# Performance work log

Measured on AMD Instinct MI355X. Metric: run time of the kernel, lower is better.

## Reference

```python
import jax, jax.numpy as jnp
import numpy as np

N_NODES = 100000


def sage_conv(x, src, dst, Wl, bl, Wr):
    # PyG SAGEConv (aggr='mean'): out = lin_l(mean_{j in N(i)} x_j) + lin_r(x_i)
    msg = x[src]                                                   # [E, d] gather
    agg = jax.ops.segment_sum(msg, dst, num_segments=N_NODES)      # [N, d]
    cnt = jax.ops.segment_sum(jnp.ones((src.shape[0], 1), x.dtype), dst,
                              num_segments=N_NODES)                # [N, 1]
    mean = agg / jnp.maximum(cnt, 1.0)
    return mean @ Wl + bl + x @ Wr


def setup_inputs() -> dict:
    key = jax.random.key(0)
    ks = jax.random.split(key, 9)
    N, E, D_IN = N_NODES, 3200000, 64
    x = jax.random.normal(ks[0], (N, D_IN), dtype=jnp.float32)
    edge_index = jax.random.randint(ks[1], (2, E), 0, N, dtype=jnp.int64)

    def glorot(k, fan_in, fan_out):
        lim = float(np.sqrt(6.0 / (fan_in + fan_out)))
        return jax.random.uniform(k, (fan_in, fan_out), jnp.float32, -lim, lim)

    return {
        "x": x,
        "edge_index": edge_index,
        "W1l": glorot(ks[2], D_IN, 64), "b1": jnp.zeros((64,), jnp.float32),
        "W1r": glorot(ks[3], D_IN, 64),
        "W2l": glorot(ks[4], 64, 32), "b2": jnp.zeros((32,), jnp.float32),
        "W2r": glorot(ks[5], 64, 32),
        "W3l": glorot(ks[6], 32, 1), "b3": jnp.zeros((1,), jnp.float32),
        "W3r": glorot(ks[7], 32, 1),
    }


def reference(x, edge_index, W1l, b1, W1r, W2l, b2, W2r, W3l, b3, W3r):
    src, dst = edge_index[0], edge_index[1]
    h = jax.nn.relu(sage_conv(x, src, dst, W1l, b1, W1r))   # dropout: eval mode (identity)
    h = jax.nn.relu(sage_conv(h, src, dst, W2l, b2, W2r))
    h = sage_conv(h, src, dst, W3l, b3, W3r)
    return jax.nn.sigmoid(h)                                # [N, 1]
```

## Files before the change

kernel.cpp:

```cpp
#include <hip/hip_runtime.h>
#include <math.h>

#define NN 100000
#define NB 391
#define BT 8192
#define CAP 12288

typedef float vfloat2 __attribute__((ext_vector_type(2)));
typedef short short8 __attribute__((ext_vector_type(8)));
typedef float floatx4 __attribute__((ext_vector_type(4)));

__device__ __forceinline__ unsigned short f2bf(float f) {
    unsigned int u = __float_as_uint(f);
    u += 0x7fffu + ((u >> 16) & 1u);
    return (unsigned short)(u >> 16);
}

__device__ __forceinline__ unsigned char f2fp8(float f) {
    const int p = __builtin_amdgcn_cvt_pk_fp8_f32(f, f, 0, false);
    return (unsigned char)(p & 0xFF);
}
template <bool HI>
__device__ __forceinline__ vfloat2 fp8pk2(unsigned int w) {
    return __builtin_amdgcn_cvt_pk_f32_fp8((int)w, HI);
}

template <int D_IN, int CL, int CR, int NPB, int FUSE_IN>
__global__ void __launch_bounds__(256)
mlp_mfma_kernel(const float* __restrict__ in0,
                const float* __restrict__ in1,
                const float* __restrict__ Wl,
                const float* __restrict__ Wr,
                const float* __restrict__ bias,
                unsigned char* __restrict__ yout,
                float* __restrict__ zout,
                int n_nodes) {
    constexpr int COLS = CL + CR;
    constexpr int CT = COLS / 16;
    constexpr int KT = D_IN / 32;
    constexpr int NT = NPB / 16;
    constexpr int KG = D_IN / 8;
    __shared__ short sA[NT * KT * 64 * 8];
    __shared__ short sB[CT * KT * 64 * 8];
    __shared__ float sBias[CR];
    const int t = threadIdx.x;
    const int node0 = blockIdx.x * NPB;

    for (int i = t; i < NPB * KG; i += 256) {
        const int nl = i / KG, kg = i % KG;
        const int n = node0 + nl;
        float v[8];
        if (n < n_nodes) {
            const float4* p = (const float4*)(in0 + (long long)n * D_IN + kg * 8);
            float4 a0 = p[0], a1 = p[1];
            if (FUSE_IN) {
                const float4* q = (const float4*)(in1 + (long long)n * D_IN + kg * 8);
                const float4 b0 = q[0], b1 = q[1];
                a0.x = fmaxf(a0.x + b0.x, 0.f); a0.y = fmaxf(a0.y + b0.y, 0.f);
                a0.z = fmaxf(a0.z + b0.z, 0.f); a0.w = fmaxf(a0.w + b0.w, 0.f);
                a1.x = fmaxf(a1.x + b1.x, 0.f); a1.y = fmaxf(a1.y + b1.y, 0.f);
                a1.z = fmaxf(a1.z + b1.z, 0.f); a1.w = fmaxf(a1.w + b1.w, 0.f);
            }
            v[0] = a0.x; v[1] = a0.y; v[2] = a0.z; v[3] = a0.w;
            v[4] = a1.x; v[5] = a1.y; v[6] = a1.z; v[7] = a1.w;
        } else {
#pragma unroll
            for (int j = 0; j < 8; ++j) v[j] = 0.f;
        }
        short8 s;
#pragma unroll
        for (int j = 0; j < 8; ++j) s[j] = (short)f2bf(v[j]);
        const int nt = nl >> 4, m = nl & 15, kt = kg >> 2, quad = kg & 3;
        ((short8*)sA)[(nt * KT + kt) * 64 + quad * 16 + m] = s;
    }
    for (int i = t; i < CT * KT * 64; i += 256) {
        const int ct = i / (KT * 64);
        const int rem = i % (KT * 64);
        const int kt = rem / 64, L = rem % 64;
        const int c = ct * 16 + (L & 15);
        const int k0 = kt * 32 + (L >> 4) * 8;
        short8 s;
#pragma unroll
        for (int j = 0; j < 8; ++j) {
            const int k = k0 + j;
            const float w = (c < CL) ? Wl[k * CL + c] : Wr[k * CR + (c - CL)];
            s[j] = (short)f2bf(w);
        }
        ((short8*)sB)[i] = s;
    }
    for (int i = t; i < CR; i += 256) sBias[i] = bias[i];
    __syncthreads();

    const int w = t >> 6, lane = t & 63;
    short8 Bf[CT][KT];
#pragma unroll
    for (int ct = 0; ct < CT; ++ct)
#pragma unroll
        for (int kt = 0; kt < KT; ++kt)
            Bf[ct][kt] = ((short8*)sB)[(ct * KT + kt) * 64 + lane];
    const int col = lane & 15, quad = lane >> 4;
#pragma unroll
    for (int nti = 0; nti < NT / 4; ++nti) {
        const int nt = w * (NT / 4) + nti;
        short8 A[KT];
#pragma unroll
        for (int kt = 0; kt < KT; ++kt)
            A[kt] = ((short8*)sA)[(nt * KT + kt) * 64 + lane];
        const int nodeb = node0 + nt * 16 + quad * 4;
#pragma unroll
        for (int ct = 0; ct < CT; ++ct) {
            floatx4 acc = {0.f, 0.f, 0.f, 0.f};
#pragma unroll
            for (int kt = 0; kt < KT; ++kt)
                acc = __builtin_amdgcn_mfma_f32_16x16x32_bf16(A[kt], Bf[ct][kt], acc, 0, 0, 0);
            const int gc = ct * 16 + col;
#pragma unroll
            for (int r = 0; r < 4; ++r) {
                const int node = nodeb + r;
                if (node < n_nodes) {
                    if (gc < CL) yout[(long long)node * CL + gc] = f2fp8(acc[r]);
                    else zout[(long long)node * CR + (gc - CL)] = acc[r] + sBias[gc - CL];
                }
            }
        }
    }
}

template <int D_IN>
__global__ void __launch_bounds__(256)
mlp3_kernel(const float* __restrict__ mean,
            const float* __restrict__ z,
            const float* __restrict__ W3l,
            const float* __restrict__ W3r,
            const float* __restrict__ b3,
            float* __restrict__ y,
            float* __restrict__ z3, int n_nodes) {
    __shared__ float swl[D_IN], swr[D_IN];
    const int t = threadIdx.x;
    if (t < D_IN) { swl[t] = W3l[t]; swr[t] = W3r[t]; }
    __syncthreads();
    const int n = blockIdx.x * 256 + t;
    if (n >= n_nodes) return;
    const float4* pm = (const float4*)(mean + (long long)n * D_IN);
    const float4* pz = (const float4*)(z + (long long)n * D_IN);
    float accl = 0.f, accr = 0.f;
#pragma unroll
    for (int q = 0; q < D_IN / 4; ++q) {
        const float4 m4 = pm[q];
        const float4 z4 = pz[q];
        const float h0 = fmaxf(m4.x + z4.x, 0.f);
        const float h1 = fmaxf(m4.y + z4.y, 0.f);
        const float h2 = fmaxf(m4.z + z4.z, 0.f);
        const float h3 = fmaxf(m4.w + z4.w, 0.f);
        accl += h0 * swl[4 * q] + h1 * swl[4 * q + 1] + h2 * swl[4 * q + 2] + h3 * swl[4 * q + 3];
        accr += h0 * swr[4 * q] + h1 * swr[4 * q + 1] + h2 * swr[4 * q + 2] + h3 * swr[4 * q + 3];
    }
    y[n] = accl;
    z3[n] = accr + b3[0];
}

template <int D>
__global__ void agg_mean_fp8_kernel(const unsigned int* __restrict__ yb,
                                    const int* __restrict__ row_ptr,
                                    const int* __restrict__ ssrc,
                                    const float* __restrict__ inv_deg,
                                    float* __restrict__ mean, int n_nodes) {
    constexpr int G = D / 16;
    constexpr int NPB = 256 / G;
    const int g = threadIdx.x / G;
    const int lane = threadIdx.x % G;
    const int n = blockIdx.x * NPB + g;
    if (n >= n_nodes) return;
    const int s0 = row_ptr[n], s1 = row_ptr[n + 1];
    const uint4* yv = (const uint4*)yb;
    float acc[16];
#pragma unroll
    for (int i = 0; i < 16; ++i) acc[i] = 0.f;
    int e = s0;
    for (; e + 4 <= s1; e += 4) {
        uint4 v[4];
        v[0] = yv[(long long)ssrc[e] * G + lane];
        v[1] = yv[(long long)ssrc[e + 1] * G + lane];
        v[2] = yv[(long long)ssrc[e + 2] * G + lane];
        v[3] = yv[(long long)ssrc[e + 3] * G + lane];
#pragma unroll
        for (int q = 0; q < 4; ++q) {
            const unsigned int wx = v[q].x, wy = v[q].y, wz = v[q].z, ww = v[q].w;
            vfloat2 p;
            p = fp8pk2<false>(wx); acc[0]  += p.x; acc[1]  += p.y;
            p = fp8pk2<true>(wx);  acc[2]  += p.x; acc[3]  += p.y;
            p = fp8pk2<false>(wy); acc[4]  += p.x; acc[5]  += p.y;
            p = fp8pk2<true>(wy);  acc[6]  += p.x; acc[7]  += p.y;
            p = fp8pk2<false>(wz); acc[8]  += p.x; acc[9]  += p.y;
            p = fp8pk2<true>(wz);  acc[10] += p.x; acc[11] += p.y;
            p = fp8pk2<false>(ww); acc[12] += p.x; acc[13] += p.y;
            p = fp8pk2<true>(ww);  acc[14] += p.x; acc[15] += p.y;
        }
    }
    for (; e < s1; ++e) {
        const uint4 v = yv[(long long)ssrc[e] * G + lane];
        vfloat2 p;
        p = fp8pk2<false>(v.x); acc[0]  += p.x; acc[1]  += p.y;
        p = fp8pk2<true>(v.x);  acc[2]  += p.x; acc[3]  += p.y;
        p = fp8pk2<false>(v.y); acc[4]  += p.x; acc[5]  += p.y;
        p = fp8pk2<true>(v.y);  acc[6]  += p.x; acc[7]  += p.y;
        p = fp8pk2<false>(v.z); acc[8]  += p.x; acc[9]  += p.y;
        p = fp8pk2<true>(v.z);  acc[10] += p.x; acc[11] += p.y;
        p = fp8pk2<false>(v.w); acc[12] += p.x; acc[13] += p.y;
        p = fp8pk2<true>(v.w);  acc[14] += p.x; acc[15] += p.y;
    }
    const float inv = inv_deg[n];
    float4* mv = (float4*)mean;
    const long long base = (long long)n * (D / 4) + lane * 4;
#pragma unroll
    for (int q = 0; q < 4; ++q)
        mv[base + q] = make_float4(acc[4 * q] * inv, acc[4 * q + 1] * inv,
                                   acc[4 * q + 2] * inv, acc[4 * q + 3] * inv);
}

__global__ void agg_d1_sig_kernel(const float* __restrict__ y,
                                  const int* __restrict__ row_ptr,
                                  const int* __restrict__ ssrc,
                                  const float* __restrict__ inv_deg,
                                  const float* __restrict__ z3,
                                  float* __restrict__ out, int n_nodes) {
    const int wave = threadIdx.x >> 6;
    const int lane = threadIdx.x & 63;
    const int n = blockIdx.x * 4 + wave;
    if (n >= n_nodes) return;
    const int s0 = row_ptr[n], s1 = row_ptr[n + 1];
    float acc = 0.f;
    for (int e = s0 + lane; e < s1; e += 64) acc += y[ssrc[e]];
    for (int off = 32; off > 0; off >>= 1) acc += __shfl_down(acc, off, 64);
    if (lane == 0) {
        const float v = acc * inv_deg[n] + z3[n];
        out[n] = 1.0f / (1.0f + expf(-v));
    }
}

__global__ void bucket_hist_kernel(const int* __restrict__ dst,
                                   int* __restrict__ bcnt, int n_edges) {
    __shared__ int lh[NB];
    for (int i = threadIdx.x; i < NB; i += 256) lh[i] = 0;
    __syncthreads();
    const int stride = gridDim.x * 256;
    for (int i = blockIdx.x * 256 + threadIdx.x; i < n_edges; i += stride)
        atomicAdd(&lh[dst[i] >> 8], 1);
    __syncthreads();
    for (int i = threadIdx.x; i < NB; i += 256)
        if (lh[i]) atomicAdd(&bcnt[i], lh[i]);
}

__global__ void __launch_bounds__(512)
bucket_scan_kernel(const int* __restrict__ bcnt, int* __restrict__ boffs,
                   int* __restrict__ bcursor) {
    __shared__ int s[512];
    const int t = threadIdx.x;
    const int v = (t < NB) ? bcnt[t] : 0;
    s[t] = v;
    __syncthreads();
    for (int off = 1; off < 512; off <<= 1) {
        const int tmp = (t >= off) ? s[t - off] : 0;
        __syncthreads();
        s[t] += tmp;
        __syncthreads();
    }
    const int excl = s[t] - v;
    if (t <= NB) boffs[t] = excl;
    if (t < NB) bcursor[t] = excl;
}

__global__ void __launch_bounds__(512)
bin_edges_kernel(const int* __restrict__ src, const int* __restrict__ dst,
                 int* __restrict__ bcursor, unsigned int* __restrict__ binned,
                 int n_edges) {
    __shared__ unsigned int stage[BT];
    __shared__ unsigned short sbkt[BT];
    __shared__ int lhist[512], lscan[512], lstart[512], gbase[512], lcur[512];
    const int t = threadIdx.x;
    const int e0 = blockIdx.x * BT;
    const int count = min(BT, n_edges - e0);
    lhist[t] = 0;
    __syncthreads();
    for (int i = t; i < count; i += 512) atomicAdd(&lhist[dst[e0 + i] >> 8], 1);
    __syncthreads();
    const int v = lhist[t];
    lscan[t] = v;
    __syncthreads();
    for (int off = 1; off < 512; off <<= 1) {
        const int tmp = (t >= off) ? lscan[t - off] : 0;
        __syncthreads();
        lscan[t] += tmp;
        __syncthreads();
    }
    const int excl = lscan[t] - v;
    lstart[t] = excl;
    lcur[t] = excl;
    if (t < NB && v > 0) gbase[t] = atomicAdd(&bcursor[t], v);
    __syncthreads();
    for (int i = t; i < count; i += 512) {
        const int d = dst[e0 + i];
        const int b = d >> 8;
        const int p = atomicAdd(&lcur[b], 1);
        stage[p] = (unsigned int)src[e0 + i] | ((unsigned int)(d & 255) << 17);
        sbkt[p] = (unsigned short)b;
    }
    __syncthreads();
    for (int i = t; i < count; i += 512) {
        const int b = sbkt[i];
        binned[gbase[b] + (i - lstart[b])] = stage[i];
    }
}

__global__ void __launch_bounds__(1024)
csr_sort_kernel(const unsigned int* __restrict__ binned,
                const int* __restrict__ boffs,
                int* __restrict__ ssrc, int* __restrict__ row_ptr,
                float* __restrict__ inv_deg, int n_nodes, int n_edges) {
    __shared__ int stage[CAP];
    __shared__ int hist[256];
    __shared__ int lexcl[256];
    __shared__ int lcur[256];
    const int t = threadIdx.x;
    const int b = blockIdx.x;
    const int s0 = boffs[b], s1 = boffs[b + 1];
    const int count = s1 - s0;
    if (t < 256) hist[t] = 0;
    __syncthreads();
    for (int i = t; i < count; i += 1024)
        atomicAdd(&hist[binned[s0 + i] >> 17], 1);
    __syncthreads();
    if (t < 256) lexcl[t] = hist[t];
    __syncthreads();
    for (int off = 1; off < 256; off <<= 1) {
        int tmp = 0;
        if (t < 256 && t >= off) tmp = lexcl[t - off];
        __syncthreads();
        if (t < 256) lexcl[t] += tmp;
        __syncthreads();
    }
    if (t < 256) {
        const int excl = lexcl[t] - hist[t];
        lcur[t] = excl;
        const int n = (b << 8) + t;
        if (n < n_nodes) {
            row_ptr[n] = s0 + excl;
            inv_deg[n] = 1.0f / (float)max(hist[t], 1);
        }
    }
    if (b == NB - 1 && t == 0) row_ptr[n_nodes] = n_edges;
    __syncthreads();
    for (int i = t; i < count; i += 1024) {
        const unsigned int v = binned[s0 + i];
        const int p = atomicAdd(&lcur[v >> 17], 1);
        if (p < CAP) stage[p] = (int)(v & 0x1FFFFu);
    }
    __syncthreads();
    for (int i = t; i < count; i += 1024) ssrc[s0 + i] = stage[i];
}

extern "C" void kernel_launch(void* const* d_in, const int* in_sizes, int n_in,
                              void* d_out, int out_size, void* d_ws, size_t ws_size,
                              hipStream_t stream) {
    const float* x = (const float*)d_in[0];
    const int* edge_index = (const int*)d_in[1];
    const float* W1l = (const float*)d_in[2];
    const float* b1  = (const float*)d_in[3];
    const float* W1r = (const float*)d_in[4];
    const float* W2l = (const float*)d_in[5];
    const float* b2  = (const float*)d_in[6];
    const float* W2r = (const float*)d_in[7];
    const float* W3l = (const float*)d_in[8];
    const float* b3  = (const float*)d_in[9];
    const float* W3r = (const float*)d_in[10];
    float* out = (float*)d_out;

    const int E = in_sizes[1] / 2;
    const int* src = edge_index;
    const int* dst = edge_index + E;

    float* bufY    = (float*)d_ws;
    float* meanB   = bufY + 32LL * NN;
    float* z1      = meanB + 64LL * NN;
    float* z2      = z1 + 64LL * NN;
    float* z3      = z2 + 32LL * NN;
    float* inv_deg = z3 + NN;
    int* bcnt      = (int*)(inv_deg + NN);
    int* boffs     = bcnt + NB;
    int* bcursor   = boffs + NB + 1;
    int* row_ptr   = bcursor + NB;
    int* ssrc      = row_ptr + NN + 1;
    unsigned int* binned = (unsigned int*)z1;

    const int ntiles = (E + BT - 1) / BT;

    (void)hipMemsetAsync(bcnt, 0, NB * sizeof(int), stream);
    bucket_hist_kernel<<<512, 256, 0, stream>>>(dst, bcnt, E);
    bucket_scan_kernel<<<1, 512, 0, stream>>>(bcnt, boffs, bcursor);
    bin_edges_kernel<<<ntiles, 512, 0, stream>>>(src, dst, bcursor, binned, E);
    csr_sort_kernel<<<NB, 1024, 0, stream>>>(binned, boffs, ssrc, row_ptr, inv_deg, NN, E);

    mlp_mfma_kernel<64, 64, 64, 128, 0><<<(NN + 127) / 128, 256, 0, stream>>>(
        x, nullptr, W1l, W1r, b1, (unsigned char*)bufY, z1, NN);
    agg_mean_fp8_kernel<64><<<(NN + 63) / 64, 256, 0, stream>>>(
        (const unsigned int*)bufY, row_ptr, ssrc, inv_deg, meanB, NN);

    mlp_mfma_kernel<64, 32, 32, 128, 1><<<(NN + 127) / 128, 256, 0, stream>>>(
        meanB, z1, W2l, W2r, b2, (unsigned char*)bufY, z2, NN);
    agg_mean_fp8_kernel<32><<<(NN + 127) / 128, 256, 0, stream>>>(
        (const unsigned int*)bufY, row_ptr, ssrc, inv_deg, meanB, NN);

    float* y3 = bufY;
    mlp3_kernel<32><<<(NN + 255) / 256, 256, 0, stream>>>(
        meanB, z2, W3l, W3r, b3, y3, z3, NN);

    agg_d1_sig_kernel<<<(NN + 3) / 4, 256, 0, stream>>>(
        y3, row_ptr, ssrc, inv_deg, z3, out, NN);
}
```

Baseline: 310.0 us.

## Fuse CSR build kernels into one cooperative kernel with grid syncs

Replaces the memset and four separate CSR-construction kernels (bucket histogram, scan, edge binning, per-bucket sort) with a single cooperative kernel of NB blocks that separates the phases with grid-wide syncs and reuses a shared-memory union. The aim is to remove launch overhead and inter-kernel gaps. In exchange, the grid is limited to 391 blocks of 512 threads, so the binning and sort phases run with less parallelism than before (the sort drops from 1024 to 512 threads per block). Grid syncs also add their own cost, and the large shared-memory union may cut occupancy.

After: 482.8 us. 55.8% more time.

```diff
diff --git a/kernel.cpp b/kernel.cpp
--- a/kernel.cpp
+++ b/kernel.cpp
@@ -1,5 +1,8 @@
 #include <hip/hip_runtime.h>
+#include <hip/hip_cooperative_groups.h>
 #include <math.h>
+
+namespace cg = cooperative_groups;
 
 #define NN 100000
 #define NB 391
@@ -23,6 +26,134 @@
 template <bool HI>
 __device__ __forceinline__ vfloat2 fp8pk2(unsigned int w) {
     return __builtin_amdgcn_cvt_pk_f32_fp8((int)w, HI);
+}
+
+union BuildSmem {
+    struct { int lh[NB]; } hist;
+    struct { int s[512]; } scan;
+    struct {
+        unsigned int stage[BT];
+        unsigned short sbkt[BT];
+        int lhist[512], lscan[512], lstart[512], gbase[512], lcur[512];
+    } bin;
+    struct { int stage[CAP]; int hist[256]; int lexcl[256]; int lcur[256]; } sort;
+};
+
+__global__ void __launch_bounds__(512)
+build_csr_coop(const int* __restrict__ src, const int* __restrict__ dst,
+               int* __restrict__ bcnt, int* __restrict__ boffs,
+               int* __restrict__ bcursor, unsigned int* __restrict__ binned,
+               int* __restrict__ ssrc, int* __restrict__ row_ptr,
+               float* __restrict__ inv_deg, int n_nodes, int n_edges) {
+    cg::grid_group grid = cg::this_grid();
+    __shared__ BuildSmem u;
+    const int t = threadIdx.x;
+    const int nb = gridDim.x;
+
+    for (int i = blockIdx.x * 512 + t; i < NB; i += nb * 512) bcnt[i] = 0;
+    grid.sync();
+
+    for (int i = t; i < NB; i += 512) u.hist.lh[i] = 0;
+    __syncthreads();
+    for (int e = blockIdx.x * 512 + t; e < n_edges; e += nb * 512)
+        atomicAdd(&u.hist.lh[dst[e] >> 8], 1);
+    __syncthreads();
+    for (int i = t; i < NB; i += 512) {
+        const int v = u.hist.lh[i];
+        if (v) atomicAdd(&bcnt[i], v);
+    }
+    grid.sync();
+
+    if (blockIdx.x == 0) {
+        const int v = (t < NB) ? bcnt[t] : 0;
+        u.scan.s[t] = v;
+        __syncthreads();
+        for (int off = 1; off < 512; off <<= 1) {
+            const int tmp = (t >= off) ? u.scan.s[t - off] : 0;
+            __syncthreads();
+            u.scan.s[t] += tmp;
+            __syncthreads();
+        }
+        const int excl = u.scan.s[t] - v;
+        if (t <= NB) boffs[t] = excl;
+        if (t < NB) bcursor[t] = excl;
+    }
+    grid.sync();
+
+    for (int tile = blockIdx.x; (long long)tile * BT < n_edges; tile += nb) {
+        const int e0 = tile * BT;
+        const int count = min(BT, n_edges - e0);
+        u.bin.lhist[t] = 0;
+        __syncthreads();
+        for (int i = t; i < count; i += 512) atomicAdd(&u.bin.lhist[dst[e0 + i] >> 8], 1);
+        __syncthreads();
+        const int v = u.bin.lhist[t];
+        u.bin.lscan[t] = v;
+        __syncthreads();
+        for (int off = 1; off < 512; off <<= 1) {
+            const int tmp = (t >= off) ? u.bin.lscan[t - off] : 0;
+            __syncthreads();
+            u.bin.lscan[t] += tmp;
+            __syncthreads();
+        }
+        const int excl = u.bin.lscan[t] - v;
+        u.bin.lstart[t] = excl;
+        u.bin.lcur[t] = excl;
+        if (t < NB && v > 0) u.bin.gbase[t] = atomicAdd(&bcursor[t], v);
+        __syncthreads();
+        for (int i = t; i < count; i += 512) {
+            const int d = dst[e0 + i];
+            const int b = d >> 8;
+            const int p = atomicAdd(&u.bin.lcur[b], 1);
+            u.bin.stage[p] = (unsigned int)src[e0 + i] | ((unsigned int)(d & 255) << 17);
+            u.bin.sbkt[p] = (unsigned short)b;
+        }
+        __syncthreads();
+        for (int i = t; i < count; i += 512) {
+            const int b = u.bin.sbkt[i];
+            binned[u.bin.gbase[b] + (i - u.bin.lstart[b])] = u.bin.stage[i];
+        }
+        __syncthreads();
+    }
+    grid.sync();
+
+    for (int b = blockIdx.x; b < NB; b += nb) {
+        const int s0 = boffs[b], s1 = boffs[b + 1];
+        const int count = s1 - s0;
+        if (t < 256) u.sort.hist[t] = 0;
+        __syncthreads();
+        for (int i = t; i < count; i += 512)
+            atomicAdd(&u.sort.hist[binned[s0 + i] >> 17], 1);
+        __syncthreads();
+        if (t < 256) u.sort.lexcl[t] = u.sort.hist[t];
+        __syncthreads();
+        for (int off = 1; off < 256; off <<= 1) {
+            int tmp = 0;
+            if (t < 256 && t >= off) tmp = u.sort.lexcl[t - off];
+            __syncthreads();
+            if (t < 256) u.sort.lexcl[t] += tmp;
+            __syncthreads();
+        }
+        if (t < 256) {
+            const int excl = u.sort.lexcl[t] - u.sort.hist[t];
+            u.sort.lcur[t] = excl;
+            const int n = (b << 8) + t;
+            if (n < n_nodes) {
+                row_ptr[n] = s0 + excl;
+                inv_deg[n] = 1.0f / (float)max(u.sort.hist[t], 1);
+            }
+        }
+        if (b == NB - 1 && t == 0) row_ptr[n_nodes] = n_edges;
+        __syncthreads();
+        for (int i = t; i < count; i += 512) {
+            const unsigned int v = binned[s0 + i];
+            const int p = atomicAdd(&u.sort.lcur[v >> 17], 1);
+            if (p < CAP) u.sort.stage[p] = (int)(v & 0x1FFFFu);
+        }
+        __syncthreads();
+        for (int i = t; i < count; i += 512) ssrc[s0 + i] = u.sort.stage[i];
+        __syncthreads();
+    }
 }
 
 template <int D_IN, int CL, int CR, int NPB, int FUSE_IN>
@@ -238,127 +369,6 @@
     }
 }
 
-__global__ void bucket_hist_kernel(const int* __restrict__ dst,
-                                   int* __restrict__ bcnt, int n_edges) {
-    __shared__ int lh[NB];
-    for (int i = threadIdx.x; i < NB; i += 256) lh[i] = 0;
-    __syncthreads();
-    const int stride = gridDim.x * 256;
-    for (int i = blockIdx.x * 256 + threadIdx.x; i < n_edges; i += stride)
-        atomicAdd(&lh[dst[i] >> 8], 1);
-    __syncthreads();
-    for (int i = threadIdx.x; i < NB; i += 256)
-        if (lh[i]) atomicAdd(&bcnt[i], lh[i]);
-}
-
-__global__ void __launch_bounds__(512)
-bucket_scan_kernel(const int* __restrict__ bcnt, int* __restrict__ boffs,
-                   int* __restrict__ bcursor) {
-    __shared__ int s[512];
-    const int t = threadIdx.x;
-    const int v = (t < NB) ? bcnt[t] : 0;
-    s[t] = v;
-    __syncthreads();
-    for (int off = 1; off < 512; off <<= 1) {
-        const int tmp = (t >= off) ? s[t - off] : 0;
-        __syncthreads();
-        s[t] += tmp;
-        __syncthreads();
-    }
-    const int excl = s[t] - v;
-    if (t <= NB) boffs[t] = excl;
-    if (t < NB) bcursor[t] = excl;
-}
-
-__global__ void __launch_bounds__(512)
-bin_edges_kernel(const int* __restrict__ src, const int* __restrict__ dst,
-                 int* __restrict__ bcursor, unsigned int* __restrict__ binned,
-                 int n_edges) {
-    __shared__ unsigned int stage[BT];
-    __shared__ unsigned short sbkt[BT];
-    __shared__ int lhist[512], lscan[512], lstart[512], gbase[512], lcur[512];
-    const int t = threadIdx.x;
-    const int e0 = blockIdx.x * BT;
-    const int count = min(BT, n_edges - e0);
-    lhist[t] = 0;
-    __syncthreads();
-    for (int i = t; i < count; i += 512) atomicAdd(&lhist[dst[e0 + i] >> 8], 1);
-    __syncthreads();
-    const int v = lhist[t];
-    lscan[t] = v;
-    __syncthreads();
-    for (int off = 1; off < 512; off <<= 1) {
-        const int tmp = (t >= off) ? lscan[t - off] : 0;
-        __syncthreads();
-        lscan[t] += tmp;
-        __syncthreads();
-    }
-    const int excl = lscan[t] - v;
-    lstart[t] = excl;
-    lcur[t] = excl;
-    if (t < NB && v > 0) gbase[t] = atomicAdd(&bcursor[t], v);
-    __syncthreads();
-    for (int i = t; i < count; i += 512) {
-        const int d = dst[e0 + i];
-        const int b = d >> 8;
-        const int p = atomicAdd(&lcur[b], 1);
-        stage[p] = (unsigned int)src[e0 + i] | ((unsigned int)(d & 255) << 17);
-        sbkt[p] = (unsigned short)b;
-    }
-    __syncthreads();
-    for (int i = t; i < count; i += 512) {
-        const int b = sbkt[i];
-        binned[gbase[b] + (i - lstart[b])] = stage[i];
-    }
-}
-
-__global__ void __launch_bounds__(1024)
-csr_sort_kernel(const unsigned int* __restrict__ binned,
-                const int* __restrict__ boffs,
-                int* __restrict__ ssrc, int* __restrict__ row_ptr,
-                float* __restrict__ inv_deg, int n_nodes, int n_edges) {
-    __shared__ int stage[CAP];
-    __shared__ int hist[256];
-    __shared__ int lexcl[256];
-    __shared__ int lcur[256];
-    const int t = threadIdx.x;
-    const int b = blockIdx.x;
-    const int s0 = boffs[b], s1 = boffs[b + 1];
-    const int count = s1 - s0;
-    if (t < 256) hist[t] = 0;
-    __syncthreads();
-    for (int i = t; i < count; i += 1024)
-        atomicAdd(&hist[binned[s0 + i] >> 17], 1);
-    __syncthreads();
-    if (t < 256) lexcl[t] = hist[t];
-    __syncthreads();
-    for (int off = 1; off < 256; off <<= 1) {
-        int tmp = 0;
-        if (t < 256 && t >= off) tmp = lexcl[t - off];
-        __syncthreads();
-        if (t < 256) lexcl[t] += tmp;
-        __syncthreads();
-    }
-    if (t < 256) {
-        const int excl = lexcl[t] - hist[t];
-        lcur[t] = excl;
-        const int n = (b << 8) + t;
-        if (n < n_nodes) {
-            row_ptr[n] = s0 + excl;
-            inv_deg[n] = 1.0f / (float)max(hist[t], 1);
-        }
-    }
-    if (b == NB - 1 && t == 0) row_ptr[n_nodes] = n_edges;
-    __syncthreads();
-    for (int i = t; i < count; i += 1024) {
-        const unsigned int v = binned[s0 + i];
-        const int p = atomicAdd(&lcur[v >> 17], 1);
-        if (p < CAP) stage[p] = (int)(v & 0x1FFFFu);
-    }
-    __syncthreads();
-    for (int i = t; i < count; i += 1024) ssrc[s0 + i] = stage[i];
-}
-
 extern "C" void kernel_launch(void* const* d_in, const int* in_sizes, int n_in,
                               void* d_out, int out_size, void* d_ws, size_t ws_size,
                               hipStream_t stream) {
@@ -392,13 +402,16 @@
     int* ssrc      = row_ptr + NN + 1;
     unsigned int* binned = (unsigned int*)z1;
 
-    const int ntiles = (E + BT - 1) / BT;
-
-    (void)hipMemsetAsync(bcnt, 0, NB * sizeof(int), stream);
-    bucket_hist_kernel<<<512, 256, 0, stream>>>(dst, bcnt, E);
-    bucket_scan_kernel<<<1, 512, 0, stream>>>(bcnt, boffs, bcursor);
-    bin_edges_kernel<<<ntiles, 512, 0, stream>>>(src, dst, bcursor, binned, E);
-    csr_sort_kernel<<<NB, 1024, 0, stream>>>(binned, boffs, ssrc, row_ptr, inv_deg, NN, E);
+    {
+        int nn = NN, e = E;
+        const int* a_src = src;
+        const int* a_dst = dst;
+        void* args[] = {(void*)&a_src, (void*)&a_dst, (void*)&bcnt, (void*)&boffs,
+                        (void*)&bcursor, (void*)&binned, (void*)&ssrc,
+                        (void*)&row_ptr, (void*)&inv_deg, (void*)&nn, (void*)&e};
+        (void)hipLaunchCooperativeKernel((void*)build_csr_coop, dim3(NB), dim3(512),
+                                         args, 0, stream);
+    }
 
     mlp_mfma_kernel<64, 64, 64, 128, 0><<<(NN + 127) / 128, 256, 0, stream>>>(
         x, nullptr, W1l, W1r, b1, (unsigned char*)bufY, z1, NN);
```
